# Optimization experiments

Measured on AMD Instinct MI355X. Metric: run time of the kernel, lower is better.

Reference implementation:

```python
import jax, jax.numpy as jnp
import numpy as np
import math

D_MODEL = 64
X_KS = 32   # input_kernel_size
Y_KS = 32   # output_kernel_size
HIDDEN = 256


def pos_enc(pos, d_model=D_MODEL):
    # standard interleaved sinusoidal encoding indexed by integer position
    i = jnp.arange(d_model // 2, dtype=jnp.float32)
    inv_freq = jnp.power(jnp.float32(10000.0), -(2.0 * i) / d_model)
    ang = pos.astype(jnp.float32)[:, None] * inv_freq[None, :]      # [N, d/2]
    pe = jnp.stack([jnp.sin(ang), jnp.cos(ang)], axis=-1)           # [N, d/2, 2]
    return pe.reshape(pos.shape[0], d_model)


def setup_inputs() -> dict:
    key = jax.random.key(0)
    ks = jax.random.split(key, 9)
    B, IN = 64, 1024
    d_in_w = 2 * D_MODEL + X_KS   # 160
    d_in_b = D_MODEL + Y_KS       # 96
    def lin(k, fan_in, fan_out):
        s = 1.0 / math.sqrt(fan_in)
        return jax.random.uniform(k, (fan_in, fan_out), jnp.float32, -s, s)
    return {
        "x": jax.random.normal(ks[0], (B, IN), jnp.float32),
        "output_size": 1024,
        "W1": lin(ks[1], d_in_w, HIDDEN), "b1": jnp.zeros((HIDDEN,), jnp.float32),
        "W2": lin(ks[2], HIDDEN, X_KS * Y_KS), "b2": jnp.zeros((X_KS * Y_KS,), jnp.float32),
        "Wb1": lin(ks[3], d_in_b, HIDDEN), "bb1": jnp.zeros((HIDDEN,), jnp.float32),
        "Wb2": lin(ks[4], HIDDEN, Y_KS), "bb2": jnp.zeros((Y_KS,), jnp.float32),
    }


def reference(x, output_size, W1, b1, W2, b2, Wb1, bb1, Wb2, bb2):
    B, input_size = x.shape
    gen_x = math.ceil(output_size / Y_KS)
    gen_y = math.ceil(input_size / X_KS)

    # pad x up to gen_y*X_KS and chunk into kernel windows, tiled gen_x times
    new_x = jnp.pad(x, ((0, 0), (0, gen_y * X_KS - input_size)))
    new_x = new_x.reshape(B, gen_y, X_KS)
    new_x = jnp.tile(new_x, (1, gen_x, 1))                          # [B, gx*gy, X_KS]

    arg_x = jnp.tile(jnp.arange(gen_x), gen_y)                      # [gx*gy]
    arg_y = jnp.repeat(jnp.arange(gen_y), gen_x)                    # [gx*gy]
    pe_x = jnp.broadcast_to(pos_enc(arg_x)[None], (B, gen_x * gen_y, D_MODEL))
    pe_y = jnp.broadcast_to(pos_enc(arg_y)[None], (B, gen_x * gen_y, D_MODEL))

    argument = jnp.concatenate([pe_x, pe_y, new_x], axis=2)         # [B, G, 2d+X_KS]

    # hypernetwork generates per-sample weight matrix
    h = jnp.tanh(argument @ W1 + b1)
    w = h @ W2 + b2                                                 # [B, G, X_KS*Y_KS]
    weight = w.reshape(B, gen_y * X_KS, gen_x * Y_KS)[:, :input_size, :output_size]

    out = jnp.einsum("bi,bio->bo", x, weight)                       # [B, output_size]

    # bias hypernetwork
    out_pad = jnp.pad(out, ((0, 0), (0, gen_x * Y_KS - output_size)))
    out_pad = out_pad.reshape(B, gen_x, Y_KS)
    pe_b = jnp.broadcast_to(pos_enc(jnp.arange(gen_x))[None], (B, gen_x, D_MODEL))
    hb = jnp.tanh(jnp.concatenate([out_pad, pe_b], axis=2) @ Wb1 + bb1)
    bias = (hb @ Wb2 + bb2).reshape(B, -1)[:, :output_size]

    return out + bias
```

## Files before the change

kernel.cpp:

```cpp
#include <hip/hip_runtime.h>
#include <math.h>

constexpr int B    = 64;
constexpr int IN   = 1024;
constexpr int OUTN = 1024;
constexpr int H    = 256;

#define LN10000 9.210340371976184f
#define TWO_LOG2E 2.8853900817779268f

__device__ __forceinline__ float fast_tanh(float x) {
    x = fminf(fmaxf(x, -15.0f), 15.0f);
    float e = __builtin_amdgcn_exp2f(x * TWO_LOG2E);
    return 1.0f - 2.0f * __builtin_amdgcn_rcpf(e + 1.0f);
}

__global__ void __launch_bounds__(256) k0_tables(const float* __restrict__ W1,
                                                 const float* __restrict__ b1,
                                                 const float* __restrict__ Wb1,
                                                 const float* __restrict__ bb1,
                                                 float* __restrict__ PA,
                                                 float* __restrict__ PY,
                                                 float* __restrict__ HPE) {
    __shared__ float pe[64];
    const int blk = blockIdx.x, tid = threadIdx.x;
    const int p = blk & 31, table = blk >> 5;
    if (tid < 32) {
        float freq = expf(-(2.0f * (float)tid / 64.0f) * LN10000);
        float a = (float)p * freq;
        pe[2 * tid]     = sinf(a);
        pe[2 * tid + 1] = cosf(a);
    }
    __syncthreads();
    const float* src; float acc; float* dst;
    if (table == 0)      { src = W1;           acc = b1[tid];  dst = PA;  }
    else if (table == 1) { src = W1 + 64 * H;  acc = 0.0f;     dst = PY;  }
    else                 { src = Wb1 + 32 * H; acc = bb1[tid]; dst = HPE; }
    #pragma unroll 16
    for (int d = 0; d < 64; ++d) acc += pe[d] * src[d * H + tid];
    dst[p * H + tid] = acc;
}

__global__ void __launch_bounds__(1024, 4) k1_v(const float* __restrict__ x,
                                                const float* __restrict__ W1,
                                                const float* __restrict__ PA,
                                                const float* __restrict__ PY,
                                                float* __restrict__ v,
                                                float* __restrict__ S) {
    __shared__ float xs[1024];
    __shared__ float w1s[2048];
    __shared__ float As[2048];
    __shared__ float red[1024];
    const int blk = blockIdx.x, tid = threadIdx.x;
    const int b = blk >> 2, cq = blk & 3, c0 = cq * 64;
    const int cl = tid & 63, jg = tid >> 6, p0 = jg * 2;

    xs[tid] = x[b * IN + tid];
    #pragma unroll
    for (int i = 0; i < 2; ++i) {
        const int idx = i * 1024 + tid;
        const int p = idx >> 6, c = idx & 63;
        w1s[idx] = W1[(128 + p) * H + c0 + c];
    }
    float acc0 = PA[p0 * H + c0 + cl];
    float acc1 = PA[(p0 + 1) * H + c0 + cl];
    const float py0 = PY[p0 * H + c0 + cl];
    const float py1 = PY[(p0 + 1) * H + c0 + cl];
    __syncthreads();

    if (cq == 0 && tid < 64) {
        float s = 0.0f;
        #pragma unroll
        for (int i = 0; i < 16; ++i) s += xs[tid + i * 64];
        #pragma unroll
        for (int off = 32; off > 0; off >>= 1) s += __shfl_xor(s, off, 64);
        if (tid == 0) S[b] = s;
    }

    {
        const float4* x0 = (const float4*)(xs + p0 * 32);
        const float4* x1 = (const float4*)(xs + (p0 + 1) * 32);
        #pragma unroll
        for (int q8 = 0; q8 < 8; ++q8) {
            float4 a4 = x0[q8], b4 = x1[q8];
            const float w0 = w1s[(q8 * 4 + 0) * 64 + cl];
            const float w1 = w1s[(q8 * 4 + 1) * 64 + cl];
            const float w2 = w1s[(q8 * 4 + 2) * 64 + cl];
            const float w3 = w1s[(q8 * 4 + 3) * 64 + cl];
            acc0 += a4.x * w0; acc1 += b4.x * w0;
            acc0 += a4.y * w1; acc1 += b4.y * w1;
            acc0 += a4.z * w2; acc1 += b4.z * w2;
            acc0 += a4.w * w3; acc1 += b4.w * w3;
        }
    }
    As[p0 * 64 + cl]       = acc0;
    As[(p0 + 1) * 64 + cl] = acc1;
    __syncthreads();

    float Areg[32];
    #pragma unroll
    for (int jx = 0; jx < 32; ++jx) Areg[jx] = As[jx * 64 + cl];
    float acc = 0.0f;
    #pragma unroll
    for (int r = 0; r < 2; ++r) {
        const float pyv = r ? py1 : py0;
        const float4* xr = (const float4*)(xs + (p0 + r) * 32);
        #pragma unroll
        for (int q8 = 0; q8 < 8; ++q8) {
            float4 xv = xr[q8];
            acc += xv.x * fast_tanh(Areg[q8 * 4 + 0] + pyv);
            acc += xv.y * fast_tanh(Areg[q8 * 4 + 1] + pyv);
            acc += xv.z * fast_tanh(Areg[q8 * 4 + 2] + pyv);
            acc += xv.w * fast_tanh(Areg[q8 * 4 + 3] + pyv);
        }
    }
    red[tid] = acc;
    __syncthreads();
    if (tid < 64) {
        float s = 0.0f;
        #pragma unroll
        for (int g = 0; g < 16; ++g) s += red[g * 64 + tid];
        v[b * H + c0 + tid] = s;
    }
}

__global__ void __launch_bounds__(1024) k2_out(const float* __restrict__ v,
                                               const float* __restrict__ S,
                                               const float* __restrict__ W2,
                                               const float* __restrict__ b2,
                                               const float* __restrict__ Wb1,
                                               const float* __restrict__ HPE,
                                               const float* __restrict__ Wb2,
                                               const float* __restrict__ bb2,
                                               float* __restrict__ out) {
    __shared__ float vsh[2048];
    __shared__ float hpe[256];
    __shared__ float osp[1024];
    __shared__ float os[256];
    __shared__ float hbs[2048];
    __shared__ float Wb2s[8192];
    __shared__ float bp[1024];
    __shared__ float Ssh[8];
    const int blk = blockIdx.x, tid = threadIdx.x;
    const int og = blk & 31, bg = blk >> 5, b0 = bg * 8;
    const int h = tid >> 8, u = tid & 255, bl = u >> 5, ol = u & 31;

    ((float2*)vsh)[tid] = ((const float2*)(v + b0 * H))[tid];
    #pragma unroll
    for (int i = 0; i < 2; ++i)
        ((float4*)Wb2s)[i * 1024 + tid] = ((const float4*)Wb2)[i * 1024 + tid];
    if (tid < 256) hpe[tid] = HPE[og * H + tid];
    if (tid < 8) Ssh[tid] = S[b0 + tid];
    __syncthreads();

    const int o = og * 32 + ol;
    {
        float acc = (h == 0) ? Ssh[bl] * b2[o] : 0.0f;
        const float4* vr = (const float4*)(vsh + bl * H + h * 64);
        #pragma unroll
        for (int c4 = 0; c4 < 16; ++c4) {
            float4 v4 = vr[c4];
            const int c = h * 64 + c4 * 4;
            acc += v4.x * W2[(c + 0) * OUTN + o];
            acc += v4.y * W2[(c + 1) * OUTN + o];
            acc += v4.z * W2[(c + 2) * OUTN + o];
            acc += v4.w * W2[(c + 3) * OUTN + o];
        }
        osp[h * 256 + u] = acc;
    }
    __syncthreads();
    if (tid < 256)
        os[tid] = osp[tid] + osp[256 + tid] + osp[512 + tid] + osp[768 + tid];
    __syncthreads();
    {
        float a0 = hpe[h * 64 + ol];
        float a1 = hpe[h * 64 + 32 + ol];
        const float4* osr = (const float4*)(os + bl * 32);
        #pragma unroll
        for (int k4 = 0; k4 < 8; ++k4) {
            float4 o4 = osr[k4];
            const float* wr = Wb1 + (k4 * 4) * H + h * 64 + ol;
            a0 += o4.x * wr[0];         a1 += o4.x * wr[32];
            a0 += o4.y * wr[H];         a1 += o4.y * wr[H + 32];
            a0 += o4.z * wr[2 * H];     a1 += o4.z * wr[2 * H + 32];
            a0 += o4.w * wr[3 * H];     a1 += o4.w * wr[3 * H + 32];
        }
        hbs[bl * H + h * 64 + ol]      = fast_tanh(a0);
        hbs[bl * H + h * 64 + 32 + ol] = fast_tanh(a1);
    }
    __syncthreads();
    {
        float bias = (h == 0) ? bb2[ol] : 0.0f;
        const float4* hr = (const float4*)(hbs + bl * H + h * 64);
        #pragma unroll
        for (int c4 = 0; c4 < 16; ++c4) {
            float4 h4 = hr[c4];
            const int c = h * 64 + c4 * 4;
            bias += h4.x * Wb2s[(c + 0) * 32 + ol];
            bias += h4.y * Wb2s[(c + 1) * 32 + ol];
            bias += h4.z * Wb2s[(c + 2) * 32 + ol];
            bias += h4.w * Wb2s[(c + 3) * 32 + ol];
        }
        bp[h * 256 + u] = bias;
    }
    __syncthreads();
    if (tid < 256) {
        out[(b0 + (tid >> 5)) * OUTN + og * 32 + (tid & 31)] =
            os[tid] + bp[tid] + bp[256 + tid] + bp[512 + tid] + bp[768 + tid];
    }
}

extern "C" void kernel_launch(void* const* d_in, const int* in_sizes, int n_in,
                              void* d_out, int out_size, void* d_ws, size_t ws_size,
                              hipStream_t stream) {
    const float* x   = (const float*)d_in[0];
    const float* W1  = (const float*)d_in[2];
    const float* b1  = (const float*)d_in[3];
    const float* W2  = (const float*)d_in[4];
    const float* b2  = (const float*)d_in[5];
    const float* Wb1 = (const float*)d_in[6];
    const float* bb1 = (const float*)d_in[7];
    const float* Wb2 = (const float*)d_in[8];
    const float* bb2 = (const float*)d_in[9];
    float* out = (float*)d_out;

    float* v   = (float*)d_ws;
    float* S   = v + B * H;
    float* PA  = S + B;
    float* PY  = PA + 32 * H;
    float* HPE = PY + 32 * H;

    hipLaunchKernelGGL(k0_tables, dim3(96),    dim3(256),  0, stream,
                       W1, b1, Wb1, bb1, PA, PY, HPE);
    hipLaunchKernelGGL(k1_v,      dim3(B * 4), dim3(1024), 0, stream,
                       x, W1, PA, PY, v, S);
    hipLaunchKernelGGL(k2_out,    dim3(256),   dim3(1024), 0, stream,
                       v, S, W2, b2, Wb1, HPE, Wb2, bb2, out);
}
```

Baseline: 89.56 us.

## Fuse positional-encoding table kernel into the two main kernels

Removes the separate k0_tables launch. The positional-encoding projections are now recomputed inside each block: kA rebuilds PA/PY from sin/cos tables in LDS, and kB rebuilds the bias PE projection. This drops one kernel launch and the global round-trip through the workspace. In exchange every block repeats that work, kA uses much more LDS (about 80KB with launch bounds dropped to 2 waves), which may reduce occupancy, and each thread runs extra sin/cos/exp.

```diff
diff --git a/kernel.cpp b/kernel.cpp
--- a/kernel.cpp
+++ b/kernel.cpp
@@ -15,40 +15,15 @@
     return 1.0f - 2.0f * __builtin_amdgcn_rcpf(e + 1.0f);
 }
 
-__global__ void __launch_bounds__(256) k0_tables(const float* __restrict__ W1,
-                                                 const float* __restrict__ b1,
-                                                 const float* __restrict__ Wb1,
-                                                 const float* __restrict__ bb1,
-                                                 float* __restrict__ PA,
-                                                 float* __restrict__ PY,
-                                                 float* __restrict__ HPE) {
-    __shared__ float pe[64];
-    const int blk = blockIdx.x, tid = threadIdx.x;
-    const int p = blk & 31, table = blk >> 5;
-    if (tid < 32) {
-        float freq = expf(-(2.0f * (float)tid / 64.0f) * LN10000);
-        float a = (float)p * freq;
-        pe[2 * tid]     = sinf(a);
-        pe[2 * tid + 1] = cosf(a);
-    }
-    __syncthreads();
-    const float* src; float acc; float* dst;
-    if (table == 0)      { src = W1;           acc = b1[tid];  dst = PA;  }
-    else if (table == 1) { src = W1 + 64 * H;  acc = 0.0f;     dst = PY;  }
-    else                 { src = Wb1 + 32 * H; acc = bb1[tid]; dst = HPE; }
-    #pragma unroll 16
-    for (int d = 0; d < 64; ++d) acc += pe[d] * src[d * H + tid];
-    dst[p * H + tid] = acc;
-}
-
-__global__ void __launch_bounds__(1024, 4) k1_v(const float* __restrict__ x,
-                                                const float* __restrict__ W1,
-                                                const float* __restrict__ PA,
-                                                const float* __restrict__ PY,
-                                                float* __restrict__ v,
-                                                float* __restrict__ S) {
+__global__ void __launch_bounds__(1024, 2) kA(const float* __restrict__ x,
+                                              const float* __restrict__ W1,
+                                              const float* __restrict__ b1,
+                                              float* __restrict__ v,
+                                              float* __restrict__ S) {
     __shared__ float xs[1024];
+    __shared__ float w1cols[8192];
     __shared__ float w1s[2048];
+    __shared__ float pe32[2048];
     __shared__ float As[2048];
     __shared__ float red[1024];
     const int blk = blockIdx.x, tid = threadIdx.x;
@@ -57,15 +32,24 @@
 
     xs[tid] = x[b * IN + tid];
     #pragma unroll
+    for (int i = 0; i < 8; ++i) {
+        const int idx = i * 1024 + tid;
+        w1cols[idx] = W1[(idx >> 6) * H + c0 + (idx & 63)];
+    }
+    #pragma unroll
     for (int i = 0; i < 2; ++i) {
         const int idx = i * 1024 + tid;
-        const int p = idx >> 6, c = idx & 63;
-        w1s[idx] = W1[(128 + p) * H + c0 + c];
-    }
-    float acc0 = PA[p0 * H + c0 + cl];
-    float acc1 = PA[(p0 + 1) * H + c0 + cl];
-    const float py0 = PY[p0 * H + c0 + cl];
-    const float py1 = PY[(p0 + 1) * H + c0 + cl];
+        w1s[idx] = W1[(128 + (idx >> 6)) * H + c0 + (idx & 63)];
+    }
+    #pragma unroll
+    for (int i = 0; i < 2; ++i) {
+        const int idx = i * 1024 + tid;
+        const int p = idx >> 6, dd = idx & 63, ii = dd >> 1;
+        float freq = expf(-(2.0f * (float)ii / 64.0f) * LN10000);
+        float a = (float)p * freq;
+        pe32[idx] = (dd & 1) ? cosf(a) : sinf(a);
+    }
+    const float b1v = b1[c0 + cl];
     __syncthreads();
 
     if (cq == 0 && tid < 64) {
@@ -75,6 +59,17 @@
         #pragma unroll
         for (int off = 32; off > 0; off >>= 1) s += __shfl_xor(s, off, 64);
         if (tid == 0) S[b] = s;
+    }
+
+    float acc0 = b1v, acc1 = b1v, py0 = 0.0f, py1 = 0.0f;
+    #pragma unroll 16
+    for (int d = 0; d < 64; ++d) {
+        const float pe0 = pe32[p0 * 64 + d];
+        const float pe1 = pe32[(p0 + 1) * 64 + d];
+        const float wA  = w1cols[d * 64 + cl];
+        const float wY  = w1cols[(64 + d) * 64 + cl];
+        acc0 += pe0 * wA;  acc1 += pe1 * wA;
+        py0  += pe0 * wY;  py1  += pe1 * wY;
     }
 
     {
@@ -124,16 +119,17 @@
     }
 }
 
-__global__ void __launch_bounds__(1024) k2_out(const float* __restrict__ v,
-                                               const float* __restrict__ S,
-                                               const float* __restrict__ W2,
-                                               const float* __restrict__ b2,
-                                               const float* __restrict__ Wb1,
-                                               const float* __restrict__ HPE,
-                                               const float* __restrict__ Wb2,
-                                               const float* __restrict__ bb2,
-                                               float* __restrict__ out) {
+__global__ void __launch_bounds__(1024) kB(const float* __restrict__ v,
+                                           const float* __restrict__ S,
+                                           const float* __restrict__ W2,
+                                           const float* __restrict__ b2,
+                                           const float* __restrict__ Wb1,
+                                           const float* __restrict__ bb1,
+                                           const float* __restrict__ Wb2,
+                                           const float* __restrict__ bb2,
+                                           float* __restrict__ out) {
     __shared__ float vsh[2048];
+    __shared__ float pes[64];
     __shared__ float hpe[256];
     __shared__ float osp[1024];
     __shared__ float os[256];
@@ -149,11 +145,24 @@
     #pragma unroll
     for (int i = 0; i < 2; ++i)
         ((float4*)Wb2s)[i * 1024 + tid] = ((const float4*)Wb2)[i * 1024 + tid];
-    if (tid < 256) hpe[tid] = HPE[og * H + tid];
+    if (tid < 64) {
+        float freq = expf(-(2.0f * (float)(tid >> 1) / 64.0f) * LN10000);
+        float a = (float)og * freq;
+        pes[tid] = (tid & 1) ? cosf(a) : sinf(a);
+    }
     if (tid < 8) Ssh[tid] = S[b0 + tid];
     __syncthreads();
 
     const int o = og * 32 + ol;
+    {
+        float hp = (h == 0) ? bb1[u] : 0.0f;
+        #pragma unroll
+        for (int dq = 0; dq < 16; ++dq) {
+            const int d = h * 16 + dq;
+            hp += pes[d] * Wb1[(32 + d) * H + u];
+        }
+        bp[h * 256 + u] = hp;
+    }
     {
         float acc = (h == 0) ? Ssh[bl] * b2[o] : 0.0f;
         const float4* vr = (const float4*)(vsh + bl * H + h * 64);
@@ -171,6 +180,10 @@
     __syncthreads();
     if (tid < 256)
         os[tid] = osp[tid] + osp[256 + tid] + osp[512 + tid] + osp[768 + tid];
+    else if (tid < 512) {
+        const int u2 = tid - 256;
+        hpe[u2] = bp[u2] + bp[256 + u2] + bp[512 + u2] + bp[768 + u2];
+    }
     __syncthreads();
     {
         float a0 = hpe[h * 64 + ol];
@@ -224,16 +237,10 @@
     const float* bb2 = (const float*)d_in[9];
     float* out = (float*)d_out;
 
-    float* v   = (float*)d_ws;
-    float* S   = v + B * H;
-    float* PA  = S + B;
-    float* PY  = PA + 32 * H;
-    float* HPE = PY + 32 * H;
-
-    hipLaunchKernelGGL(k0_tables, dim3(96),    dim3(256),  0, stream,
-                       W1, b1, Wb1, bb1, PA, PY, HPE);
-    hipLaunchKernelGGL(k1_v,      dim3(B * 4), dim3(1024), 0, stream,
-                       x, W1, PA, PY, v, S);
-    hipLaunchKernelGGL(k2_out,    dim3(256),   dim3(1024), 0, stream,
-                       v, S, W2, b2, Wb1, HPE, Wb2, bb2, out);
-}
+    float* v = (float*)d_ws;
+    float* S = v + B * H;
+
+    hipLaunchKernelGGL(kA, dim3(B * 4), dim3(1024), 0, stream, x, W1, b1, v, S);
+    hipLaunchKernelGGL(kB, dim3(256),   dim3(1024), 0, stream,
+                       v, S, W2, b2, Wb1, bb1, Wb2, bb2, out);
+}
```

Result: slower. 91.54 us (+2.2%).
